# Kernel tuning notes

Measured on AMD Instinct MI355X. Metric: run time of the kernel, lower is better.

The kernel has to match this reference:

```python
import jax, jax.numpy as jnp
import numpy as np

N_NODES = 100000
N_EDGES = 800000
F_IN, N_HID, N_CLS = 256, 128, 40


def setup_inputs() -> dict:
    key = jax.random.key(0)
    ks = jax.random.split(key, 6)
    features = jax.random.normal(ks[0], (N_NODES, F_IN), dtype=jnp.float32)
    src = jax.random.randint(ks[1], (N_EDGES,), 0, N_NODES, dtype=jnp.int64)
    dst = jax.random.randint(ks[2], (N_EDGES,), 0, N_NODES, dtype=jnp.int64)
    W1 = jax.random.normal(ks[3], (F_IN, N_HID), dtype=jnp.float32) / np.sqrt(F_IN)
    b1 = jnp.zeros((N_HID,), dtype=jnp.float32)
    W2 = jax.random.normal(ks[4], (N_HID, N_CLS), dtype=jnp.float32) / np.sqrt(N_HID)
    b2 = jnp.zeros((N_CLS,), dtype=jnp.float32)
    return {"features": features, "src": src, "dst": dst,
            "W1": W1, "b1": b1, "W2": W2, "b2": b2}


def reference(features, src, dst, W1, b1, W2, b2):
    # DGL GraphConv with norm='both': h = D_dst^{-1/2} A (D_src^{-1/2} x) W + b
    # Eval mode: dropout(p=0.85) is identity.
    N = features.shape[0]
    ones = jnp.ones(src.shape[0], dtype=features.dtype)
    out_deg = jax.ops.segment_sum(ones, src, num_segments=N)
    in_deg = jax.ops.segment_sum(ones, dst, num_segments=N)
    norm_src = jnp.where(out_deg > 0, out_deg ** -0.5, 0.0)[:, None]  # [N,1]
    norm_dst = jnp.where(in_deg > 0, in_deg ** -0.5, 0.0)[:, None]

    def gconv(x, W, b):
        # project first (in_feats >= out_feats here) to shrink SpMM width
        h = (x * norm_src) @ W                                # [N, out]
        agg = jax.ops.segment_sum(h[src], dst, num_segments=N)  # sparse aggregate
        return agg * norm_dst + b

    x = jax.nn.relu(gconv(features, W1, b1))
    return gconv(x, W2, b2)
```

## Files before the change

kernel.cpp:

```cpp
#include <hip/hip_runtime.h>
#include <hip/hip_bf16.h>
#include <math.h>


#define F_IN  256
#define F_HID 128
#define F_CLS 40

#define RSZ 16384
#define NSL 16

typedef __bf16 bf16_t;
typedef bf16_t bf16x8 __attribute__((ext_vector_type(8)));
typedef float floatx4 __attribute__((ext_vector_type(4)));

static __device__ __forceinline__ unsigned short f2b(float f) {
    __hip_bfloat16 h = __float2bfloat16(f);
    return __builtin_bit_cast(unsigned short, h);
}
static __device__ __forceinline__ float b2f(unsigned short u) {
    return __uint_as_float((unsigned)u << 16);
}
static __device__ __forceinline__ unsigned short f2h(float f) {
    return __builtin_bit_cast(unsigned short, (_Float16)f);
}
static __device__ __forceinline__ float h2f(unsigned short u) {
    return (float)__builtin_bit_cast(_Float16, u);
}

__global__ __launch_bounds__(256) void hist_kernel(
    const int* __restrict__ src, const int* __restrict__ dst,
    unsigned* __restrict__ partial_s, unsigned* __restrict__ partial_d, int E)
{
    __shared__ unsigned h[RSZ];
    const int t = threadIdx.x;
    const int r  = blockIdx.x / NSL;
    const int sl = blockIdx.x % NSL;
    const int lo = r * RSZ;
    const int* __restrict__ keys = blockIdx.y ? dst : src;
    unsigned* __restrict__ part = blockIdx.y ? partial_d : partial_s;

    for (int i = t; i < RSZ; i += 256) h[i] = 0;
    __syncthreads();

    const int slice = (E + NSL - 1) / NSL;
    const int e0 = sl * slice;
    const int e1 = min(E, e0 + slice);

    int e = e0 + t;
    for (; e + 7 * 256 < e1; e += 8 * 256) {
        int k[8];
        #pragma unroll
        for (int i = 0; i < 8; ++i) k[i] = keys[e + i * 256];
        #pragma unroll
        for (int i = 0; i < 8; ++i) {
            unsigned kk = (unsigned)(k[i] - lo);
            if (kk < RSZ) atomicAdd(&h[kk], 1u);
        }
    }
    for (; e < e1; e += 256) {
        unsigned kk = (unsigned)(keys[e] - lo);
        if (kk < RSZ) atomicAdd(&h[kk], 1u);
    }
    __syncthreads();

    unsigned* dst_p = part + (size_t)blockIdx.x * RSZ;
    for (int i = t; i < RSZ; i += 256) dst_p[i] = h[i];
}

__global__ __launch_bounds__(256) void scan1_kernel(
    const unsigned* __restrict__ partial_s, const unsigned* __restrict__ partial_d,
    int* __restrict__ row_off, int* __restrict__ blk_sums,
    float* __restrict__ norm_src, float* __restrict__ norm_dst, int N)
{
    __shared__ int s[256];
    const int t = threadIdx.x;
    const int base = blockIdx.x * 1024 + t * 4;

    unsigned ss0 = 0, ss1 = 0, ss2 = 0, ss3 = 0;
    unsigned sd0 = 0, sd1 = 0, sd2 = 0, sd3 = 0;
    {
        const int r = base / RSZ;
        const int off = base & (RSZ - 1);
        const unsigned* ps = partial_s + (size_t)r * NSL * RSZ + off;
        const unsigned* pd = partial_d + (size_t)r * NSL * RSZ + off;
        #pragma unroll
        for (int sl = 0; sl < NSL; ++sl) {
            uint4 a = *(const uint4*)(ps + (size_t)sl * RSZ);
            uint4 b = *(const uint4*)(pd + (size_t)sl * RSZ);
            ss0 += a.x; ss1 += a.y; ss2 += a.z; ss3 += a.w;
            sd0 += b.x; sd1 += b.y; sd2 += b.z; sd3 += b.w;
        }
    }
    if (base + 0 < N) {
        norm_src[base + 0] = ss0 ? 1.0f / sqrtf((float)ss0) : 0.0f;
        norm_dst[base + 0] = sd0 ? 1.0f / sqrtf((float)sd0) : 0.0f;
    }
    if (base + 1 < N) {
        norm_src[base + 1] = ss1 ? 1.0f / sqrtf((float)ss1) : 0.0f;
        norm_dst[base + 1] = sd1 ? 1.0f / sqrtf((float)sd1) : 0.0f;
    }
    if (base + 2 < N) {
        norm_src[base + 2] = ss2 ? 1.0f / sqrtf((float)ss2) : 0.0f;
        norm_dst[base + 2] = sd2 ? 1.0f / sqrtf((float)sd2) : 0.0f;
    }
    if (base + 3 < N) {
        norm_src[base + 3] = ss3 ? 1.0f / sqrtf((float)ss3) : 0.0f;
        norm_dst[base + 3] = sd3 ? 1.0f / sqrtf((float)sd3) : 0.0f;
    }

    int v0 = (base + 0 < N) ? (int)sd0 : 0;
    int v1 = (base + 1 < N) ? (int)sd1 : 0;
    int v2 = (base + 2 < N) ? (int)sd2 : 0;
    int v3 = (base + 3 < N) ? (int)sd3 : 0;
    int local = v0 + v1 + v2 + v3;
    s[t] = local;
    __syncthreads();
    for (int off = 1; off < 256; off <<= 1) {
        int x = (t >= off) ? s[t - off] : 0;
        __syncthreads();
        s[t] += x;
        __syncthreads();
    }
    int excl = s[t] - local;
    if (t == 255) blk_sums[blockIdx.x] = s[t];
    if (base + 0 < N) row_off[base + 0] = excl;
    if (base + 1 < N) row_off[base + 1] = excl + v0;
    if (base + 2 < N) row_off[base + 2] = excl + v0 + v1;
    if (base + 3 < N) row_off[base + 3] = excl + v0 + v1 + v2;
}

__global__ __launch_bounds__(256) void scan2_pack_kernel(
    int* __restrict__ blk_sums, int B,
    const float* __restrict__ W1, __hip_bfloat16* __restrict__ W1t)
{
    const int t = threadIdx.x;
    if (blockIdx.x > 0) {
        int idx = (blockIdx.x - 1) * 256 + t;
        int n = idx >> 8;
        int k = idx & 255;
        W1t[idx] = __float2bfloat16(W1[(size_t)k * F_HID + n]);
        return;
    }
    __shared__ int s[256];
    int local = (t < B) ? blk_sums[t] : 0;
    s[t] = local;
    __syncthreads();
    for (int off = 1; off < 256; off <<= 1) {
        int x = (t >= off) ? s[t - off] : 0;
        __syncthreads();
        s[t] += x;
        __syncthreads();
    }
    if (t < B) blk_sums[t] = s[t] - local;
}

__global__ __launch_bounds__(256) void scan3_slicepref_kernel(
    int* __restrict__ row_off, const int* __restrict__ blk_sums,
    unsigned* __restrict__ partial_d, int N, int E, int NRtot)
{
    const int idx = blockIdx.x * 256 + threadIdx.x;
    if (idx >= NRtot) return;
    unsigned run = 0;
    if (idx < N) {
        int v = row_off[idx] + blk_sums[idx >> 10];
        row_off[idx] = v;
        run = (unsigned)v;
    }
    if (idx == N) row_off[N] = E;
    const int r = idx / RSZ;
    const int i = idx & (RSZ - 1);
    unsigned* p = partial_d + (size_t)r * NSL * RSZ + i;
    #pragma unroll
    for (int sl = 0; sl < NSL; ++sl) {
        unsigned c = p[(size_t)sl * RSZ];
        p[(size_t)sl * RSZ] = run;
        run += c;
    }
}

__global__ __launch_bounds__(256) void scatter2_kernel(
    const int* __restrict__ src, const int* __restrict__ dst,
    const unsigned* __restrict__ pref, int* __restrict__ csr_src, int E)
{
    __shared__ unsigned cur[RSZ];
    const int t = threadIdx.x;
    const int r  = blockIdx.x / NSL;
    const int sl = blockIdx.x % NSL;
    const int lo = r * RSZ;
    const unsigned* p = pref + (size_t)blockIdx.x * RSZ;

    for (int i = t; i < RSZ; i += 256) cur[i] = p[i];
    __syncthreads();

    const int slice = (E + NSL - 1) / NSL;
    const int e0 = sl * slice;
    const int e1 = min(E, e0 + slice);

    int e = e0 + t;
    for (; e + 7 * 256 < e1; e += 8 * 256) {
        int d[8], s[8];
        #pragma unroll
        for (int i = 0; i < 8; ++i) { d[i] = dst[e + i * 256]; s[i] = src[e + i * 256]; }
        #pragma unroll
        for (int i = 0; i < 8; ++i) {
            unsigned k = (unsigned)(d[i] - lo);
            if (k < RSZ) {
                unsigned pos = atomicAdd(&cur[k], 1u);
                csr_src[pos] = s[i];
            }
        }
    }
    for (; e < e1; e += 256) {
        unsigned k = (unsigned)(dst[e] - lo);
        if (k < RSZ) {
            unsigned pos = atomicAdd(&cur[k], 1u);
            csr_src[pos] = src[e];
        }
    }
}

__global__ __launch_bounds__(512, 4) void gemm1_mfma_kernel(
    const float* __restrict__ X, const __hip_bfloat16* __restrict__ W1t,
    const float* __restrict__ norm_src, __hip_bfloat16* __restrict__ h1b, int N)
{
    __shared__ __hip_bfloat16 Bs[128 * 256];
    const int t = threadIdx.x;
    const int node0 = blockIdx.x * 128;
    const int lane = t & 63;
    const int w = t >> 6;
    const int l15 = lane & 15;
    const int quad = lane >> 4;

    const int arow = node0 + w * 16 + l15;
    const bool valid = arow < N;
    const int arow_c = valid ? arow : (N - 1);
    const float ns = valid ? norm_src[arow] : 0.0f;

    const float* xp = X + (size_t)arow_c * F_IN + quad * 8;

    float4 araw[4];
    araw[0] = *(const float4*)(xp + 0);
    araw[1] = *(const float4*)(xp + 4);
    araw[2] = *(const float4*)(xp + 32);
    araw[3] = *(const float4*)(xp + 36);

    #pragma unroll
    for (int i = 0; i < 8; ++i) {
        int idx = i * 512 + t;
        int row = idx >> 5;
        int ch  = idx & 31;
        uint4 v = *(const uint4*)(W1t + (size_t)row * F_IN + ch * 8);
        int d = row * 256 + ((ch * 8) ^ ((row & 7) << 3));
        *(uint4*)(Bs + d) = v;
    }
    __syncthreads();

    const int swz = (l15 & 7) << 3;
    const int bbase0 = l15 * 256 + ((quad * 8) ^ swz);
    const int bbase1 = l15 * 256 + ((32 + quad * 8) ^ swz);

    floatx4 acc[8] = {};

    #pragma unroll
    for (int c = 0; c < 4; ++c) {
        bf16x8 ab0, ab1;
        {
            union { bf16x8 v; unsigned short u[8]; } cv;
            cv.u[0] = f2b(araw[0].x * ns); cv.u[1] = f2b(araw[0].y * ns);
            cv.u[2] = f2b(araw[0].z * ns); cv.u[3] = f2b(araw[0].w * ns);
            cv.u[4] = f2b(araw[1].x * ns); cv.u[5] = f2b(araw[1].y * ns);
            cv.u[6] = f2b(araw[1].z * ns); cv.u[7] = f2b(araw[1].w * ns);
            ab0 = cv.v;
            cv.u[0] = f2b(araw[2].x * ns); cv.u[1] = f2b(araw[2].y * ns);
            cv.u[2] = f2b(araw[2].z * ns); cv.u[3] = f2b(araw[2].w * ns);
            cv.u[4] = f2b(araw[3].x * ns); cv.u[5] = f2b(araw[3].y * ns);
            cv.u[6] = f2b(araw[3].z * ns); cv.u[7] = f2b(araw[3].w * ns);
            ab1 = cv.v;
        }
        if (c < 3) {
            araw[0] = *(const float4*)(xp + (c + 1) * 64 + 0);
            araw[1] = *(const float4*)(xp + (c + 1) * 64 + 4);
            araw[2] = *(const float4*)(xp + (c + 1) * 64 + 32);
            araw[3] = *(const float4*)(xp + (c + 1) * 64 + 36);
        }
        #pragma unroll
        for (int nt = 0; nt < 8; ++nt) {
            bf16x8 b = *(const bf16x8*)(Bs + bbase0 + nt * 16 * 256 + c * 64);
            acc[nt] = __builtin_amdgcn_mfma_f32_16x16x32_bf16(ab0, b, acc[nt], 0, 0, 0);
        }
        #pragma unroll
        for (int nt = 0; nt < 8; ++nt) {
            bf16x8 b = *(const bf16x8*)(Bs + bbase1 + nt * 16 * 256 + c * 64);
            acc[nt] = __builtin_amdgcn_mfma_f32_16x16x32_bf16(ab1, b, acc[nt], 0, 0, 0);
        }
    }

    #pragma unroll
    for (int nt = 0; nt < 8; ++nt) {
        #pragma unroll
        for (int r = 0; r < 4; ++r) {
            int node = node0 + w * 16 + quad * 4 + r;
            if (node < N)
                h1b[(size_t)node * F_HID + nt * 16 + l15] = __float2bfloat16(acc[nt][r]);
        }
    }
}

__global__ __launch_bounds__(256) void spmm1_csr_kernel(
    const __hip_bfloat16* __restrict__ h1b, const int* __restrict__ row_off,
    const int* __restrict__ csr_src, const float* __restrict__ norm_src,
    const float* __restrict__ norm_dst, const float* __restrict__ b1,
    unsigned short* __restrict__ h1act, int N)
{
    const int t = threadIdx.x;
    const int node = blockIdx.x * 8 + (t >> 5);
    if (node >= N) return;
    const int c = (t & 31) << 2;
    const int start = row_off[node];
    const int end = row_off[node + 1];
    float4 acc = make_float4(0.f, 0.f, 0.f, 0.f);
    int j = start;
    for (; j + 8 <= end; j += 8) {
        int s[8];
        #pragma unroll
        for (int i = 0; i < 8; ++i) s[i] = csr_src[j + i];
        ushort4 u[8];
        #pragma unroll
        for (int i = 0; i < 8; ++i)
            u[i] = *(const ushort4*)(h1b + (size_t)s[i] * F_HID + c);
        #pragma unroll
        for (int i = 0; i < 8; ++i) {
            acc.x += b2f(u[i].x);
            acc.y += b2f(u[i].y);
            acc.z += b2f(u[i].z);
            acc.w += b2f(u[i].w);
        }
    }
    for (; j + 2 <= end; j += 2) {
        int s0 = csr_src[j + 0];
        int s1 = csr_src[j + 1];
        ushort4 u0 = *(const ushort4*)(h1b + (size_t)s0 * F_HID + c);
        ushort4 u1 = *(const ushort4*)(h1b + (size_t)s1 * F_HID + c);
        acc.x += b2f(u0.x) + b2f(u1.x);
        acc.y += b2f(u0.y) + b2f(u1.y);
        acc.z += b2f(u0.z) + b2f(u1.z);
        acc.w += b2f(u0.w) + b2f(u1.w);
    }
    if (j < end) {
        int s = csr_src[j];
        ushort4 u = *(const ushort4*)(h1b + (size_t)s * F_HID + c);
        acc.x += b2f(u.x);
        acc.y += b2f(u.y);
        acc.z += b2f(u.z);
        acc.w += b2f(u.w);
    }
    const float nd = norm_dst[node];
    const float ns = norm_src[node];
    float4 bb = *(const float4*)(b1 + c);
    ushort4 o;
    o.x = f2h(fmaxf(fmaf(acc.x, nd, bb.x), 0.f) * ns);
    o.y = f2h(fmaxf(fmaf(acc.y, nd, bb.y), 0.f) * ns);
    o.z = f2h(fmaxf(fmaf(acc.z, nd, bb.z), 0.f) * ns);
    o.w = f2h(fmaxf(fmaf(acc.w, nd, bb.w), 0.f) * ns);
    *(ushort4*)(h1act + (size_t)node * F_HID + c) = o;
}

__global__ __launch_bounds__(320) void gemm2_kernel(
    const unsigned short* __restrict__ h1act, const float* __restrict__ W2,
    unsigned short* __restrict__ h2, int N)
{
    __shared__ float As[64][132];
    __shared__ float Ws[128][40];
    const int t = threadIdx.x;
    const int node0 = blockIdx.x * 64;

    #pragma unroll
    for (int i = 0; i < 4; ++i) {
        int f = t + 320 * i;
        int r = f / 10;
        int kk = (f % 10) * 4;
        *(float4*)&Ws[r][kk] = *(const float4*)(W2 + (size_t)r * F_CLS + kk);
    }
    for (int f = t; f < 2048; f += 320) {
        int r = f >> 5;
        int kk = (f & 31) << 2;
        int node = node0 + r;
        float4 v = make_float4(0.f, 0.f, 0.f, 0.f);
        if (node < N) {
            ushort4 u = *(const ushort4*)(h1act + (size_t)node * F_HID + kk);
            v.x = h2f(u.x); v.y = h2f(u.y); v.z = h2f(u.z); v.w = h2f(u.w);
        }
        *(float4*)&As[r][kk] = v;
    }
    __syncthreads();

    const int col = t % 40;
    const int rowg = t / 40;
    float acc[8] = {};
    #pragma unroll 8
    for (int k = 0; k < F_HID; ++k) {
        float w = Ws[k][col];
        #pragma unroll
        for (int i = 0; i < 8; ++i)
            acc[i] = fmaf(As[rowg * 8 + i][k], w, acc[i]);
    }
    #pragma unroll
    for (int i = 0; i < 8; ++i) {
        int node = node0 + rowg * 8 + i;
        if (node < N) h2[(size_t)node * F_CLS + col] = f2h(acc[i]);
    }
}

__global__ __launch_bounds__(256) void spmm2_csr_kernel(
    const unsigned short* __restrict__ h2, const int* __restrict__ row_off,
    const int* __restrict__ csr_src, const float* __restrict__ norm_dst,
    const float* __restrict__ b2, float* __restrict__ out, int N)
{
    const int t = threadIdx.x;
    if (t >= 250) return;
    const int node = blockIdx.x * 25 + t / 10;
    const int lane = t % 10;
    if (node >= N) return;
    const int c = lane << 2;
    const int start = row_off[node];
    const int end = row_off[node + 1];
    float4 acc = make_float4(0.f, 0.f, 0.f, 0.f);
    int j = start;
    for (; j + 8 <= end; j += 8) {
        int s[8];
        #pragma unroll
        for (int i = 0; i < 8; ++i) s[i] = csr_src[j + i];
        ushort4 u[8];
        #pragma unroll
        for (int i = 0; i < 8; ++i)
            u[i] = *(const ushort4*)(h2 + (size_t)s[i] * F_CLS + c);
        #pragma unroll
        for (int i = 0; i < 8; ++i) {
            acc.x += h2f(u[i].x);
            acc.y += h2f(u[i].y);
            acc.z += h2f(u[i].z);
            acc.w += h2f(u[i].w);
        }
    }
    for (; j + 2 <= end; j += 2) {
        int s0 = csr_src[j + 0];
        int s1 = csr_src[j + 1];
        ushort4 u0 = *(const ushort4*)(h2 + (size_t)s0 * F_CLS + c);
        ushort4 u1 = *(const ushort4*)(h2 + (size_t)s1 * F_CLS + c);
        acc.x += h2f(u0.x) + h2f(u1.x);
        acc.y += h2f(u0.y) + h2f(u1.y);
        acc.z += h2f(u0.z) + h2f(u1.z);
        acc.w += h2f(u0.w) + h2f(u1.w);
    }
    if (j < end) {
        int s = csr_src[j];
        ushort4 u = *(const ushort4*)(h2 + (size_t)s * F_CLS + c);
        acc.x += h2f(u.x);
        acc.y += h2f(u.y);
        acc.z += h2f(u.z);
        acc.w += h2f(u.w);
    }
    float nd = norm_dst[node];
    float4 bb = *(const float4*)(b2 + c);
    float4 r;
    r.x = fmaf(acc.x, nd, bb.x);
    r.y = fmaf(acc.y, nd, bb.y);
    r.z = fmaf(acc.z, nd, bb.z);
    r.w = fmaf(acc.w, nd, bb.w);
    *(float4*)(out + (size_t)node * F_CLS + c) = r;
}

extern "C" void kernel_launch(void* const* d_in, const int* in_sizes, int n_in,
                              void* d_out, int out_size, void* d_ws, size_t ws_size,
                              hipStream_t stream) {
    const float* X   = (const float*)d_in[0];
    const int*   src = (const int*)d_in[1];
    const int*   dst = (const int*)d_in[2];
    const float* W1  = (const float*)d_in[3];
    const float* b1  = (const float*)d_in[4];
    const float* W2  = (const float*)d_in[5];
    const float* b2  = (const float*)d_in[6];
    float* out = (float*)d_out;

    const int N = in_sizes[0] / F_IN;
    const int E = in_sizes[1];
    const int NB = (N + 1023) / 1024;
    const int NR = (N + RSZ - 1) / RSZ;
    const int NRtot = NR * RSZ;

    char* w = (char*)d_ws;
    int*   row_off  = (int*)w;                      w += (size_t)(N + 4) * 4;
    int*   blk_sums = (int*)w;                      w += 256 * 4;
    int*   csr_src  = (int*)w;                      w += (size_t)E * 4;
    float* norm_src = (float*)w;                    w += (size_t)N * 4;
    float* norm_dst = (float*)w;                    w += (size_t)N * 4;
    unsigned short* h1act = (unsigned short*)w;     w += (size_t)N * F_HID * 2;
    unsigned short* h2    = (unsigned short*)w;     w += (size_t)N * F_CLS * 2;
    __hip_bfloat16* W1t = (__hip_bfloat16*)w;       w += (size_t)F_HID * F_IN * 2;
    __hip_bfloat16* h1b = (__hip_bfloat16*)w;       w += (size_t)N * F_HID * 2;
    unsigned* partial_s = (unsigned*)w;             w += (size_t)NR * NSL * RSZ * 4;
    unsigned* partial_d = (unsigned*)w;             w += (size_t)NR * NSL * RSZ * 4;

    hist_kernel<<<dim3(NR * NSL, 2), 256, 0, stream>>>(src, dst, partial_s, partial_d, E);

    scan1_kernel<<<NB, 256, 0, stream>>>(partial_s, partial_d, row_off, blk_sums,
                                         norm_src, norm_dst, N);
    scan2_pack_kernel<<<1 + (F_HID * F_IN) / 256, 256, 0, stream>>>(blk_sums, NB, W1, W1t);
    scan3_slicepref_kernel<<<(NRtot + 255) / 256, 256, 0, stream>>>(
        row_off, blk_sums, partial_d, N, E, NRtot);

    scatter2_kernel<<<NR * NSL, 256, 0, stream>>>(src, dst, partial_d, csr_src, E);

    gemm1_mfma_kernel<<<(N + 127) / 128, 512, 0, stream>>>(X, W1t, norm_src, h1b, N);

    spmm1_csr_kernel<<<(N + 7) / 8, 256, 0, stream>>>(h1b, row_off, csr_src,
                                                      norm_src, norm_dst, b1, h1act, N);

    gemm2_kernel<<<(N + 63) / 64, 320, 0, stream>>>(h1act, W2, h2, N);

    spmm2_csr_kernel<<<(N + 24) / 25, 256, 0, stream>>>(h2, row_off, csr_src, norm_dst, b2, out, N);
}
```

Before: 352.1 us.

## Fuse layer-2 projection into SpMM1 via MFMA and retune histogram slicing

The first aggregation kernel now writes its 16-node activation tile to shared memory and multiplies it by a pre-transposed fp16 W2 using MFMA inside the same kernel. This removes the separate gemm2 kernel and the round trip of the N×128 activation through global memory. W2 is transposed and padded to 48 columns inside the existing pack kernel. The histogram range and slice constants are also changed (smaller ranges, more slices). In exchange, only one wave per block does the MFMA after a block-wide barrier, and the fp16 MFMA path replaces the fp32 FMA GEMM.

After: 301.7 us, median of 2. 14.3% less time.

```diff
diff --git a/kernel.cpp b/kernel.cpp
--- a/kernel.cpp
+++ b/kernel.cpp
@@ -7,12 +7,13 @@
 #define F_HID 128
 #define F_CLS 40
 
-#define RSZ 16384
-#define NSL 16
+#define RSZ 8192
+#define NSL 32
 
 typedef __bf16 bf16_t;
 typedef bf16_t bf16x8 __attribute__((ext_vector_type(8)));
 typedef float floatx4 __attribute__((ext_vector_type(4)));
+typedef _Float16 f16x8 __attribute__((ext_vector_type(8)));
 
 static __device__ __forceinline__ unsigned short f2b(float f) {
     __hip_bfloat16 h = __float2bfloat16(f);
@@ -132,9 +133,17 @@
 
 __global__ __launch_bounds__(256) void scan2_pack_kernel(
     int* __restrict__ blk_sums, int B,
-    const float* __restrict__ W1, __hip_bfloat16* __restrict__ W1t)
-{
-    const int t = threadIdx.x;
+    const float* __restrict__ W1, __hip_bfloat16* __restrict__ W1t,
+    const float* __restrict__ W2, unsigned short* __restrict__ W2t)
+{
+    const int t = threadIdx.x;
+    if (blockIdx.x > 128) {
+        int idx = (blockIdx.x - 129) * 256 + t;
+        int n = idx >> 7;
+        int k = idx & 127;
+        W2t[idx] = (n < F_CLS) ? f2h(W2[(size_t)k * F_CLS + n]) : (unsigned short)0;
+        return;
+    }
     if (blockIdx.x > 0) {
         int idx = (blockIdx.x - 1) * 256 + t;
         int n = idx >> 8;
@@ -307,108 +316,97 @@
     }
 }
 
-__global__ __launch_bounds__(256) void spmm1_csr_kernel(
+__global__ __launch_bounds__(512) void spmm1_fused_kernel(
     const __hip_bfloat16* __restrict__ h1b, const int* __restrict__ row_off,
     const int* __restrict__ csr_src, const float* __restrict__ norm_src,
     const float* __restrict__ norm_dst, const float* __restrict__ b1,
-    unsigned short* __restrict__ h1act, int N)
-{
-    const int t = threadIdx.x;
-    const int node = blockIdx.x * 8 + (t >> 5);
-    if (node >= N) return;
+    const unsigned short* __restrict__ W2t, unsigned short* __restrict__ h2, int N)
+{
+    __shared__ unsigned short As[16][136];
+    const int t = threadIdx.x;
+    const int g = t >> 5;
+    const int node = blockIdx.x * 16 + g;
     const int c = (t & 31) << 2;
-    const int start = row_off[node];
-    const int end = row_off[node + 1];
-    float4 acc = make_float4(0.f, 0.f, 0.f, 0.f);
-    int j = start;
-    for (; j + 8 <= end; j += 8) {
-        int s[8];
-        #pragma unroll
-        for (int i = 0; i < 8; ++i) s[i] = csr_src[j + i];
-        ushort4 u[8];
-        #pragma unroll
-        for (int i = 0; i < 8; ++i)
-            u[i] = *(const ushort4*)(h1b + (size_t)s[i] * F_HID + c);
-        #pragma unroll
-        for (int i = 0; i < 8; ++i) {
-            acc.x += b2f(u[i].x);
-            acc.y += b2f(u[i].y);
-            acc.z += b2f(u[i].z);
-            acc.w += b2f(u[i].w);
-        }
-    }
-    for (; j + 2 <= end; j += 2) {
-        int s0 = csr_src[j + 0];
-        int s1 = csr_src[j + 1];
-        ushort4 u0 = *(const ushort4*)(h1b + (size_t)s0 * F_HID + c);
-        ushort4 u1 = *(const ushort4*)(h1b + (size_t)s1 * F_HID + c);
-        acc.x += b2f(u0.x) + b2f(u1.x);
-        acc.y += b2f(u0.y) + b2f(u1.y);
-        acc.z += b2f(u0.z) + b2f(u1.z);
-        acc.w += b2f(u0.w) + b2f(u1.w);
-    }
-    if (j < end) {
-        int s = csr_src[j];
-        ushort4 u = *(const ushort4*)(h1b + (size_t)s * F_HID + c);
-        acc.x += b2f(u.x);
-        acc.y += b2f(u.y);
-        acc.z += b2f(u.z);
-        acc.w += b2f(u.w);
-    }
-    const float nd = norm_dst[node];
-    const float ns = norm_src[node];
-    float4 bb = *(const float4*)(b1 + c);
-    ushort4 o;
-    o.x = f2h(fmaxf(fmaf(acc.x, nd, bb.x), 0.f) * ns);
-    o.y = f2h(fmaxf(fmaf(acc.y, nd, bb.y), 0.f) * ns);
-    o.z = f2h(fmaxf(fmaf(acc.z, nd, bb.z), 0.f) * ns);
-    o.w = f2h(fmaxf(fmaf(acc.w, nd, bb.w), 0.f) * ns);
-    *(ushort4*)(h1act + (size_t)node * F_HID + c) = o;
-}
-
-__global__ __launch_bounds__(320) void gemm2_kernel(
-    const unsigned short* __restrict__ h1act, const float* __restrict__ W2,
-    unsigned short* __restrict__ h2, int N)
-{
-    __shared__ float As[64][132];
-    __shared__ float Ws[128][40];
-    const int t = threadIdx.x;
-    const int node0 = blockIdx.x * 64;
-
+
+    if (node < N) {
+        const int start = row_off[node];
+        const int end = row_off[node + 1];
+        float4 acc = make_float4(0.f, 0.f, 0.f, 0.f);
+        int j = start;
+        for (; j + 8 <= end; j += 8) {
+            int s[8];
+            #pragma unroll
+            for (int i = 0; i < 8; ++i) s[i] = csr_src[j + i];
+            ushort4 u[8];
+            #pragma unroll
+            for (int i = 0; i < 8; ++i)
+                u[i] = *(const ushort4*)(h1b + (size_t)s[i] * F_HID + c);
+            #pragma unroll
+            for (int i = 0; i < 8; ++i) {
+                acc.x += b2f(u[i].x);
+                acc.y += b2f(u[i].y);
+                acc.z += b2f(u[i].z);
+                acc.w += b2f(u[i].w);
+            }
+        }
+        for (; j + 2 <= end; j += 2) {
+            int s0 = csr_src[j + 0];
+            int s1 = csr_src[j + 1];
+            ushort4 u0 = *(const ushort4*)(h1b + (size_t)s0 * F_HID + c);
+            ushort4 u1 = *(const ushort4*)(h1b + (size_t)s1 * F_HID + c);
+            acc.x += b2f(u0.x) + b2f(u1.x);
+            acc.y += b2f(u0.y) + b2f(u1.y);
+            acc.z += b2f(u0.z) + b2f(u1.z);
+            acc.w += b2f(u0.w) + b2f(u1.w);
+        }
+        if (j < end) {
+            int s = csr_src[j];
+            ushort4 u = *(const ushort4*)(h1b + (size_t)s * F_HID + c);
+            acc.x += b2f(u.x);
+            acc.y += b2f(u.y);
+            acc.z += b2f(u.z);
+            acc.w += b2f(u.w);
+        }
+        const float nd = norm_dst[node];
+        const float ns = norm_src[node];
+        float4 bb = *(const float4*)(b1 + c);
+        ushort4 o;
+        o.x = f2h(fmaxf(fmaf(acc.x, nd, bb.x), 0.f) * ns);
+        o.y = f2h(fmaxf(fmaf(acc.y, nd, bb.y), 0.f) * ns);
+        o.z = f2h(fmaxf(fmaf(acc.z, nd, bb.z), 0.f) * ns);
+        o.w = f2h(fmaxf(fmaf(acc.w, nd, bb.w), 0.f) * ns);
+        *(ushort4*)&As[g][c] = o;
+    } else {
+        ushort4 z = make_ushort4(0, 0, 0, 0);
+        *(ushort4*)&As[g][c] = z;
+    }
+    __syncthreads();
+    if (t >= 64) return;
+
+    const int l15 = t & 15;
+    const int quad = t >> 4;
+    floatx4 co[3] = {};
     #pragma unroll
-    for (int i = 0; i < 4; ++i) {
-        int f = t + 320 * i;
-        int r = f / 10;
-        int kk = (f % 10) * 4;
-        *(float4*)&Ws[r][kk] = *(const float4*)(W2 + (size_t)r * F_CLS + kk);
-    }
-    for (int f = t; f < 2048; f += 320) {
-        int r = f >> 5;
-        int kk = (f & 31) << 2;
-        int node = node0 + r;
-        float4 v = make_float4(0.f, 0.f, 0.f, 0.f);
-        if (node < N) {
-            ushort4 u = *(const ushort4*)(h1act + (size_t)node * F_HID + kk);
-            v.x = h2f(u.x); v.y = h2f(u.y); v.z = h2f(u.z); v.w = h2f(u.w);
-        }
-        *(float4*)&As[r][kk] = v;
-    }
-    __syncthreads();
-
-    const int col = t % 40;
-    const int rowg = t / 40;
-    float acc[8] = {};
-    #pragma unroll 8
-    for (int k = 0; k < F_HID; ++k) {
-        float w = Ws[k][col];
-        #pragma unroll
-        for (int i = 0; i < 8; ++i)
-            acc[i] = fmaf(As[rowg * 8 + i][k], w, acc[i]);
-    }
+    for (int kc = 0; kc < 4; ++kc) {
+        f16x8 a = *(const f16x8*)&As[l15][kc * 32 + quad * 8];
+        #pragma unroll
+        for (int ct = 0; ct < 3; ++ct) {
+            f16x8 b = *(const f16x8*)(W2t + (size_t)(ct * 16 + l15) * F_HID
+                                          + kc * 32 + quad * 8);
+            co[ct] = __builtin_amdgcn_mfma_f32_16x16x32_f16(a, b, co[ct], 0, 0, 0);
+        }
+    }
+    const int node0 = blockIdx.x * 16;
     #pragma unroll
-    for (int i = 0; i < 8; ++i) {
-        int node = node0 + rowg * 8 + i;
-        if (node < N) h2[(size_t)node * F_CLS + col] = f2h(acc[i]);
+    for (int ct = 0; ct < 3; ++ct) {
+        int col = ct * 16 + l15;
+        if (col < F_CLS) {
+            #pragma unroll
+            for (int i = 0; i < 4; ++i) {
+                int n2 = node0 + quad * 4 + i;
+                if (n2 < N) h2[(size_t)n2 * F_CLS + col] = f2h(co[ct][i]);
+            }
+        }
     }
 }
 
@@ -495,9 +493,9 @@
     int*   csr_src  = (int*)w;                      w += (size_t)E * 4;
     float* norm_src = (float*)w;                    w += (size_t)N * 4;
     float* norm_dst = (float*)w;                    w += (size_t)N * 4;
-    unsigned short* h1act = (unsigned short*)w;     w += (size_t)N * F_HID * 2;
-    unsigned short* h2    = (unsigned short*)w;     w += (size_t)N * F_CLS * 2;
+    unsigned short* h2 = (unsigned short*)w;        w += (size_t)N * F_CLS * 2;
     __hip_bfloat16* W1t = (__hip_bfloat16*)w;       w += (size_t)F_HID * F_IN * 2;
+    unsigned short* W2t = (unsigned short*)w;       w += (size_t)48 * F_HID * 2;
     __hip_bfloat16* h1b = (__hip_bfloat16*)w;       w += (size_t)N * F_HID * 2;
     unsigned* partial_s = (unsigned*)w;             w += (size_t)NR * NSL * RSZ * 4;
     unsigned* partial_d = (unsigned*)w;             w += (size_t)NR * NSL * RSZ * 4;
@@ -506,7 +504,7 @@
 
     scan1_kernel<<<NB, 256, 0, stream>>>(partial_s, partial_d, row_off, blk_sums,
                                          norm_src, norm_dst, N);
-    scan2_pack_kernel<<<1 + (F_HID * F_IN) / 256, 256, 0, stream>>>(blk_sums, NB, W1, W1t);
+    scan2_pack_kernel<<<153, 256, 0, stream>>>(blk_sums, NB, W1, W1t, W2, W2t);
     scan3_slicepref_kernel<<<(NRtot + 255) / 256, 256, 0, stream>>>(
         row_off, blk_sums, partial_d, N, E, NRtot);
 
@@ -514,10 +512,10 @@
 
     gemm1_mfma_kernel<<<(N + 127) / 128, 512, 0, stream>>>(X, W1t, norm_src, h1b, N);
 
-    spmm1_csr_kernel<<<(N + 7) / 8, 256, 0, stream>>>(h1b, row_off, csr_src,
-                                                      norm_src, norm_dst, b1, h1act, N);
-
-    gemm2_kernel<<<(N + 63) / 64, 320, 0, stream>>>(h1act, W2, h2, N);
-
-    spmm2_csr_kernel<<<(N + 24) / 25, 256, 0, stream>>>(h2, row_off, csr_src, norm_dst, b2, out, N);
-}
+    spmm1_fused_kernel<<<(N + 15) / 16, 512, 0, stream>>>(h1b, row_off, csr_src,
+                                                          norm_src, norm_dst, b1,
+                                                          W2t, h2, N);
+
+    spmm2_csr_kernel<<<(N + 24) / 25, 256, 0, stream>>>(h2, row_off, csr_src,
+                                                        norm_dst, b2, out, N);
+}
```
